# Kernel tuning notes

Hardware: AMD Instinct MI355X
Metric: run time of the kernel (lower is better)

Reference implementation:

```python
import jax, jax.numpy as jnp
import numpy as np

T, B, DIM, N = 2048, 8, 1024, 64

def setup_inputs() -> dict:
    key = jax.random.key(0)
    ks = jax.random.split(key, 6)
    scale = 1.0 / np.sqrt(DIM)  # xavier-ish for Linear(dim, n_state)
    return {
        "x": jax.random.normal(ks[0], (T, B, DIM), dtype=jnp.float32),
        "S0": jnp.zeros((B, N, N), dtype=jnp.float32),
        "W_k": jax.random.normal(ks[1], (N, DIM), dtype=jnp.float32) * scale,
        "W_v": jax.random.normal(ks[2], (N, DIM), dtype=jnp.float32) * scale,
        "W_q": jax.random.normal(ks[3], (N, DIM), dtype=jnp.float32) * scale,
        "W_alpha": jax.random.normal(ks[4], (N, DIM), dtype=jnp.float32) * scale,
        "b_alpha": jnp.full((N,), 2.0, dtype=jnp.float32),
        "d_g": jnp.full((N,), 0.5, dtype=jnp.float32),
        "b_g": jnp.zeros((N,), dtype=jnp.float32),
    }

def reference(x, S0, W_k, W_v, W_q, W_alpha, b_alpha, d_g, b_g):
    # Precompute all projections: [T, B, N]
    k_all = jnp.einsum('tbd,nd->tbn', x, W_k)
    v_all = jnp.einsum('tbd,nd->tbn', x, W_v)
    q_all = jnp.einsum('tbd,nd->tbn', x, W_q)
    alpha_all = jax.nn.sigmoid(jnp.einsum('tbd,nd->tbn', x, W_alpha) + b_alpha)

    def step(S, inp):
        k, v, q, alpha = inp  # each [B, N]
        retrieved = jnp.einsum('bij,bj->bi', S, k)          # S @ k
        g = jax.nn.sigmoid(d_g * retrieved + b_g)
        v_gated = v * g
        outer_vk = jnp.einsum('bi,bj->bij', v_gated, k)
        S = alpha[..., None] * S + (1.0 - alpha[..., None]) * outer_vk
        out = jnp.einsum('bij,bj->bi', S, q)                # S @ q
        out = out * jax.nn.silu(out)                        # self-gate
        return S, out

    S_final, output = jax.lax.scan(step, S0, (k_all, v_all, q_all, alpha_all))
    return output, S_final
```

## Files before the change

kernel.cpp:

```cpp
#include <hip/hip_runtime.h>

#define TT 2048
#define BB 8
#define DD 1024
#define NN 64
#define C64 64
#define NC2 (TT / C64)

typedef __attribute__((ext_vector_type(8))) short bfrag;
typedef __attribute__((ext_vector_type(4))) float f32x4;
typedef __attribute__((ext_vector_type(8))) unsigned short ushort8;

__device__ __forceinline__ float rcp_(float x) { return __builtin_amdgcn_rcpf(x); }
__device__ __forceinline__ float exp2_(float x) {
#if __has_builtin(__builtin_amdgcn_exp2f)
    return __builtin_amdgcn_exp2f(x);
#else
    return exp2f(x);
#endif
}
__device__ __forceinline__ float sigmoidf_(float x) {
    return rcp_(1.0f + __expf(-x));
}
__device__ __forceinline__ float bcastlane(float x, int l) {
    return __int_as_float(__builtin_amdgcn_readlane(__float_as_int(x), l));
}

template <int CTRL, int RM>
__device__ __forceinline__ float dpp_mul1(float x) {
    int v = __builtin_amdgcn_update_dpp(
        0x3f800000, __float_as_int(x), CTRL, RM, 0xF, false);
    return x * __int_as_float(v);
}
__device__ __forceinline__ float prefix_mul64(float x) {
    x = dpp_mul1<0x111, 0xF>(x);
    x = dpp_mul1<0x112, 0xF>(x);
    x = dpp_mul1<0x114, 0xF>(x);
    x = dpp_mul1<0x118, 0xF>(x);
    x = dpp_mul1<0x142, 0xA>(x);
    x = dpp_mul1<0x143, 0xC>(x);
    return x;
}

__device__ __forceinline__ unsigned short cvt_bf16(float f) {
    unsigned int u = __float_as_uint(f);
    return (unsigned short)((u + 0x7FFF + ((u >> 16) & 1)) >> 16);
}

__device__ __forceinline__ void gll16(const float* g, float* l) {
    __builtin_amdgcn_global_load_lds(
        (const __attribute__((address_space(1))) void*)g,
        (__attribute__((address_space(3))) void*)l, 16, 0, 0);
}

__global__ __launch_bounds__(256) void wcvt_kernel(
    const float* __restrict__ W0, const float* __restrict__ W1,
    const float* __restrict__ W2, const float* __restrict__ W3,
    unsigned short* __restrict__ Wb)
{
    const int i = blockIdx.x * 256 + threadIdx.x;
    const int o = i * 8;
    const int col = o & 31;
    const int row = (o >> 5) & 63;
    const int kt  = (o >> 11) & 31;
    const int mat = o >> 16;
    const float* __restrict__ W = (mat == 0) ? W0 : (mat == 1) ? W1
                                 : (mat == 2) ? W2 : W3;
    const float* src = &W[(size_t)row * DD + kt * 32 + col];
    const float4 a = *(const float4*)src;
    const float4 b = *(const float4*)(src + 4);
    ushort8 r;
    r[0] = cvt_bf16(a.x); r[1] = cvt_bf16(a.y);
    r[2] = cvt_bf16(a.z); r[3] = cvt_bf16(a.w);
    r[4] = cvt_bf16(b.x); r[5] = cvt_bf16(b.y);
    r[6] = cvt_bf16(b.z); r[7] = cvt_bf16(b.w);
    *(ushort8*)&Wb[o] = r;
}

__global__ __launch_bounds__(256) void proj_fused_kernel(
    const float* __restrict__ x, const unsigned short* __restrict__ Wb,
    const float* __restrict__ b_alpha,
    float* __restrict__ O0, float* __restrict__ O1,
    float* __restrict__ O2, float* __restrict__ O3)
{
    const int m0   = blockIdx.x * 64;
    const int tid  = threadIdx.x;
    const int lane = tid & 63;
    const int wave = tid >> 6;
    const int ln   = lane & 15;
    const int q8   = (lane >> 4) * 8;

    __shared__ unsigned short As[64][40];
    __shared__ unsigned short Bs[4][64][40];

    f32x4 acc[4][4] = {};

    const int arow = tid >> 2;
    const int aseg = (tid & 3) * 8;

    float4 pa[2];
    ushort8 pw[4];
    {
        const float* ap = &x[(size_t)(m0 + arow) * DD + aseg];
        pa[0] = *(const float4*)ap;
        pa[1] = *(const float4*)(ap + 4);
        const ushort8* wp = (const ushort8*)&Wb[((size_t)(wave * 32 + 0) * 64 + lane) * 32];
        #pragma unroll
        for (int j = 0; j < 4; j++) pw[j] = wp[j];
    }

    for (int k0 = 0; k0 < DD; k0 += 32) {
        __syncthreads();
        {
            unsigned short t8[8];
            const float* pf = (const float*)pa;
            #pragma unroll
            for (int j = 0; j < 8; j++) t8[j] = cvt_bf16(pf[j]);
            *(ushort8*)&As[arow][aseg] = *(ushort8*)&t8[0];
            #pragma unroll
            for (int j = 0; j < 4; j++)
                *(ushort8*)&Bs[wave][lane][8 * j] = pw[j];
        }
        if (k0 + 32 < DD) {
            const int kt = (k0 >> 5) + 1;
            const float* ap = &x[(size_t)(m0 + arow) * DD + k0 + 32 + aseg];
            pa[0] = *(const float4*)ap;
            pa[1] = *(const float4*)(ap + 4);
            const ushort8* wp = (const ushort8*)&Wb[((size_t)(wave * 32 + kt) * 64 + lane) * 32];
            #pragma unroll
            for (int j = 0; j < 4; j++) pw[j] = wp[j];
        }
        __syncthreads();

        const bfrag af = *(const bfrag*)&As[wave * 16 + ln][q8];
        #pragma unroll
        for (int mat = 0; mat < 4; mat++) {
            bfrag bf[4];
            #pragma unroll
            for (int nt = 0; nt < 4; nt++)
                bf[nt] = *(const bfrag*)&Bs[mat][nt * 16 + ln][q8];
            #pragma unroll
            for (int nt = 0; nt < 4; nt++)
                acc[mat][nt] = __builtin_amdgcn_mfma_f32_16x16x32_bf16(
                    af, bf[nt], acc[mat][nt], 0, 0, 0);
        }
    }

    #pragma unroll
    for (int mat = 0; mat < 4; mat++) {
        float* __restrict__ C = (mat == 0) ? O0 : (mat == 1) ? O1
                               : (mat == 2) ? O2 : O3;
        #pragma unroll
        for (int nt = 0; nt < 4; nt++) {
            const int col = nt * 16 + ln;
            const float ba = (mat == 3) ? b_alpha[col] : 0.0f;
            #pragma unroll
            for (int r = 0; r < 4; r++) {
                const int row = m0 + wave * 16 + (lane >> 4) * 4 + r;
                float v = acc[mat][nt][r];
                if (mat == 3) v = sigmoidf_(v + ba);
                C[(size_t)row * NN + col] = v;
            }
        }
    }
}

__global__ __launch_bounds__(256) void gram_kernel(
    const float* __restrict__ k_all, const float* __restrict__ q_all,
    float* __restrict__ gkq)
{
    const int c  = blockIdx.x;
    const int b  = blockIdx.y;
    const int t0 = c * C64;
    const int tid = threadIdx.x;

    __shared__ __align__(16) float Ks[64][68];
    __shared__ __align__(16) float Qs[64][68];

    {
        const int r = tid >> 2, sg = (tid & 3) * 16;
        const float* kp = &k_all[(size_t)(t0 + r) * (BB * NN) + b * NN + sg];
        const float* qp = &q_all[(size_t)(t0 + r) * (BB * NN) + b * NN + sg];
        #pragma unroll
        for (int j = 0; j < 4; ++j) {
            *(float4*)&Ks[r][sg + 4 * j] = *(const float4*)(kp + 4 * j);
            *(float4*)&Qs[r][sg + 4 * j] = *(const float4*)(qp + 4 * j);
        }
    }
    __syncthreads();

    const int ti = tid >> 4, tj = tid & 15;
    float g[4][4] = {}, kq[4][4] = {};
    #pragma unroll
    for (int c4 = 0; c4 < 16; ++c4) {
        float4 ka[4], kb[4], qb[4];
        #pragma unroll
        for (int r = 0; r < 4; ++r) {
            ka[r] = *(const float4*)&Ks[4 * ti + r][c4 * 4];
            kb[r] = *(const float4*)&Ks[4 * tj + r][c4 * 4];
            qb[r] = *(const float4*)&Qs[4 * tj + r][c4 * 4];
        }
        #pragma unroll
        for (int r = 0; r < 4; ++r)
            #pragma unroll
            for (int q = 0; q < 4; ++q) {
                g[r][q]  = fmaf(ka[r].x, kb[q].x, g[r][q]);
                g[r][q]  = fmaf(ka[r].y, kb[q].y, g[r][q]);
                g[r][q]  = fmaf(ka[r].z, kb[q].z, g[r][q]);
                g[r][q]  = fmaf(ka[r].w, kb[q].w, g[r][q]);
                kq[r][q] = fmaf(ka[r].x, qb[q].x, kq[r][q]);
                kq[r][q] = fmaf(ka[r].y, qb[q].y, kq[r][q]);
                kq[r][q] = fmaf(ka[r].z, qb[q].z, kq[r][q]);
                kq[r][q] = fmaf(ka[r].w, qb[q].w, kq[r][q]);
            }
    }

    float* base = gkq + (size_t)(b * NC2 + c) * 64 * 128;
    #pragma unroll
    for (int r = 0; r < 4; ++r) {
        #pragma unroll
        for (int q = 0; q < 4; ++q) {
            const int t   = 4 * tj + q;
            const int pos = ((ti ^ (t & 15)) << 2) + r;
            base[t * 128 + pos]      = g[r][q];
            base[t * 128 + 64 + pos] = kq[r][q];
        }
    }
}

__global__ __launch_bounds__(128, 1) void scan_kernel(
    const float* __restrict__ gkq,
    const float* __restrict__ k_all, const float* __restrict__ q_all,
    const float* __restrict__ a_all, const float* __restrict__ v_all,
    const float* __restrict__ S0,
    const float* __restrict__ d_g, const float* __restrict__ b_g,
    float* __restrict__ out, float* __restrict__ S_final)
{
    const int b    = blockIdx.x;
    const int rg   = blockIdx.y;
    const int tid  = threadIdx.x;
    const int lane = tid & 63;
    const int wave = tid >> 6;
    const int row  = rg * 2 + wave;

    __shared__ __align__(16) float gT[2][64 * 128];
    __shared__ __align__(16) float Kl[2][64 * 64];
    __shared__ __align__(16) float Ql[2][64 * 64];
    __shared__ __align__(16) float sbuf[2][64];

    float S = S0[((size_t)b * NN + row) * NN + lane];
    const float L2E  = 1.4426950408889634f;
    const float ndg2 = -d_g[row] * L2E;
    const float nbg2 = -b_g[row] * L2E;

    const float* gkq_b = gkq + (size_t)b * NC2 * 64 * 128;

    const int s_loc = lane >> 4;
    const int gr    = lane & 15;

    auto stage = [&](int c, int db) {
        const float* src = gkq_b + (size_t)c * 64 * 128;
        #pragma unroll
        for (int j = 0; j < 16; ++j) {
            const int off = (wave * 32 + 2 * j) * 128;
            gll16(src + off + lane * 4, &gT[db][off]);
        }
        #pragma unroll
        for (int j = 0; j < 8; ++j) {
            const int r0 = wave * 32 + 4 * j;
            const int s  = r0 + s_loc;
            const int gg = gr ^ (s & 15);
            const size_t goff = ((size_t)(c * C64 + s) * BB + b) * NN + gg * 4;
            gll16(k_all + goff, &Kl[db][r0 * 64]);
            gll16(q_all + goff, &Ql[db][r0 * 64]);
        }
    };

    float a_nx, v_nx;
    auto aw_load = [&](int c) {
        const size_t goff = ((size_t)(c * C64 + lane) * BB + b) * NN + row;
        a_nx = a_all[goff];
        v_nx = v_all[goff];
    };

    stage(0, 0);
    aw_load(0);

    for (int c = 0; c < NC2; ++c) {
        const int db = c & 1;
        const float ac = a_nx;
        const float wc = (1.0f - a_nx) * v_nx;
        __syncthreads();
        if (c + 1 < NC2) { aw_load(c + 1); stage(c + 1, db ^ 1); }

        const float P  = prefix_mul64(ac);
        const float Pm = P / ac;
        const float u  = wc * rcp_(P);

        sbuf[wave][lane] = S;
        const float* Kb = &Kl[db][0];
        const float* Qb = &Ql[db][0];
        float4 ha = {0.f, 0.f, 0.f, 0.f};
        float4 hb = {0.f, 0.f, 0.f, 0.f};
        #pragma unroll
        for (int g4 = 0; g4 < 16; ++g4) {
            const int idx = lane * 64 + ((g4 ^ gr) << 2);
            float4 kv = *(const float4*)&Kb[idx];
            float4 qv = *(const float4*)&Qb[idx];
            float4 sv = *(const float4*)&sbuf[wave][g4 << 2];
            ha.x = fmaf(kv.x, sv.x, ha.x); ha.y = fmaf(kv.y, sv.y, ha.y);
            ha.z = fmaf(kv.z, sv.z, ha.z); ha.w = fmaf(kv.w, sv.w, ha.w);
            hb.x = fmaf(qv.x, sv.x, hb.x); hb.y = fmaf(qv.y, sv.y, hb.y);
            hb.z = fmaf(qv.z, sv.z, hb.z); hb.w = fmaf(qv.w, sv.w, hb.w);
        }
        const float h  = (ha.x + ha.y) + (ha.z + ha.w);
        const float hq = (hb.x + hb.y) + (hb.z + hb.w);
        const float e1 = ndg2 * Pm;
        const float e0 = fmaf(e1, h, nbg2);

        const float* gt = &gT[db][0];
        const int rowbase = lane * 128;

        float z = e0;
        float Bacc = 0.f, Bl = 0.f, slat = 0.f;

        f32x4 g2a0, g2a1, q2a0, q2a1, g2b0, g2b1, q2b0, q2b1;

#define LOADBLK(G0, G1, Q0, Q1, blk) do {                                   \
        const int j0_ = ((2 * (blk)) ^ gr) << 2;                            \
        const int j1_ = ((2 * (blk) + 1) ^ gr) << 2;                        \
        const f32x4 rg0_ = *(const f32x4*)&gt[rowbase + j0_];               \
        const f32x4 rg1_ = *(const f32x4*)&gt[rowbase + j1_];               \
        const f32x4 rq0_ = *(const f32x4*)&gt[rowbase + 64 + j0_];          \
        const f32x4 rq1_ = *(const f32x4*)&gt[rowbase + 64 + j1_];          \
        const float u0_ = bcastlane(u, 8*(blk)+0);                          \
        const float u1_ = bcastlane(u, 8*(blk)+1);                          \
        const float u2_ = bcastlane(u, 8*(blk)+2);                          \
        const float u3_ = bcastlane(u, 8*(blk)+3);                          \
        const float u4_ = bcastlane(u, 8*(blk)+4);                          \
        const float u5_ = bcastlane(u, 8*(blk)+5);                          \
        const float u6_ = bcastlane(u, 8*(blk)+6);                          \
        const float u7_ = bcastlane(u, 8*(blk)+7);                          \
        Q0[0] = rq0_[0]*u0_; Q0[1] = rq0_[1]*u1_;                           \
        Q0[2] = rq0_[2]*u2_; Q0[3] = rq0_[3]*u3_;                           \
        Q1[0] = rq1_[0]*u4_; Q1[1] = rq1_[1]*u5_;                           \
        Q1[2] = rq1_[2]*u6_; Q1[3] = rq1_[3]*u7_;                           \
        G0[0] = rg0_[0]*u0_*e1; G0[1] = rg0_[1]*u1_*e1;                     \
        G0[2] = rg0_[2]*u2_*e1; G0[3] = rg0_[3]*u3_*e1;                     \
        G1[0] = rg1_[0]*u4_*e1; G1[1] = rg1_[1]*u5_*e1;                     \
        G1[2] = rg1_[2]*u6_*e1; G1[3] = rg1_[3]*u7_*e1;                     \
    } while (0)

#define STEP1(ss, gv, qv) do {                                              \
        const float zs_ = bcastlane(z, (ss));                               \
        const float ex_ = exp2_(zs_);                                       \
        const float sg_ = rcp_(1.0f + ex_);                                 \
        z    = fmaf((gv), sg_, z);                                          \
        Bacc = fmaf((qv), sg_, Bacc);                                       \
        Bl   = (lane == (ss)) ? Bacc : Bl;                                  \
        slat = (lane == (ss)) ? sg_  : slat;                                \
    } while (0)

#define STEP8(blk, G0, G1, Q0, Q1)                                          \
        STEP1(8*(blk)+0, G0[0], Q0[0]); STEP1(8*(blk)+1, G0[1], Q0[1]);     \
        STEP1(8*(blk)+2, G0[2], Q0[2]); STEP1(8*(blk)+3, G0[3], Q0[3]);     \
        STEP1(8*(blk)+4, G1[0], Q1[0]); STEP1(8*(blk)+5, G1[1], Q1[1]);     \
        STEP1(8*(blk)+6, G1[2], Q1[2]); STEP1(8*(blk)+7, G1[3], Q1[3]);

        LOADBLK(g2a0, g2a1, q2a0, q2a1, 0);
        LOADBLK(g2b0, g2b1, q2b0, q2b1, 1);
        STEP8(0, g2a0, g2a1, q2a0, q2a1); LOADBLK(g2a0, g2a1, q2a0, q2a1, 2);
        STEP8(1, g2b0, g2b1, q2b0, q2b1); LOADBLK(g2b0, g2b1, q2b0, q2b1, 3);
        STEP8(2, g2a0, g2a1, q2a0, q2a1); LOADBLK(g2a0, g2a1, q2a0, q2a1, 4);
        STEP8(3, g2b0, g2b1, q2b0, q2b1); LOADBLK(g2b0, g2b1, q2b0, q2b1, 5);
        STEP8(4, g2a0, g2a1, q2a0, q2a1); LOADBLK(g2a0, g2a1, q2a0, q2a1, 6);
        STEP8(5, g2b0, g2b1, q2b0, q2b1); LOADBLK(g2b0, g2b1, q2b0, q2b1, 7);
        STEP8(6, g2a0, g2a1, q2a0, q2a1);
        STEP8(7, g2b0, g2b1, q2b0, q2b1);

#undef LOADBLK
#undef STEP1
#undef STEP8

        const float chl = u * slat;
        float Sa0 = 0.f, Sa1 = 0.f, Sa2 = 0.f, Sa3 = 0.f;
        #pragma unroll
        for (int s = 0; s < 64; s += 4) {
            const float c0 = bcastlane(chl, s);
            const float c1 = bcastlane(chl, s + 1);
            const float c2 = bcastlane(chl, s + 2);
            const float c3 = bcastlane(chl, s + 3);
            const int sw = ((lane >> 2) << 2);
            Sa0 = fmaf(c0, Kb[(s)     * 64 + ((sw ^ (((s)     & 15) << 2))) + (lane & 3)], Sa0);
            Sa1 = fmaf(c1, Kb[(s + 1) * 64 + ((sw ^ (((s + 1) & 15) << 2))) + (lane & 3)], Sa1);
            Sa2 = fmaf(c2, Kb[(s + 2) * 64 + ((sw ^ (((s + 2) & 15) << 2))) + (lane & 3)], Sa2);
            Sa3 = fmaf(c3, Kb[(s + 3) * 64 + ((sw ^ (((s + 3) & 15) << 2))) + (lane & 3)], Sa3);
        }
        const float Sa = (Sa0 + Sa1) + (Sa2 + Sa3);

        const float o = P * (hq + Bl);
        const float y = o * o * rcp_(1.0f + exp2_(-o * L2E));
        out[((size_t)(c * C64 + lane) * BB + b) * NN + row] = y;
        const float Pl = bcastlane(P, 63);
        S = Pl * (S + Sa);
    }

    S_final[((size_t)b * NN + row) * NN + lane] = S;
}

extern "C" void kernel_launch(void* const* d_in, const int* in_sizes, int n_in,
                              void* d_out, int out_size, void* d_ws, size_t ws_size,
                              hipStream_t stream) {
    const float* x       = (const float*)d_in[0];
    const float* S0      = (const float*)d_in[1];
    const float* W_k     = (const float*)d_in[2];
    const float* W_v     = (const float*)d_in[3];
    const float* W_q     = (const float*)d_in[4];
    const float* W_alpha = (const float*)d_in[5];
    const float* b_alpha = (const float*)d_in[6];
    const float* d_g     = (const float*)d_in[7];
    const float* b_g     = (const float*)d_in[8];
    float* out = (float*)d_out;

    const size_t arr = (size_t)TT * BB * NN;
    float* ws    = (float*)d_ws;
    float* k_all = ws;
    float* v_all = ws + arr;
    float* q_all = ws + 2 * arr;
    float* a_all = ws + 3 * arr;
    float* gkq   = ws + 4 * arr;
    unsigned short* Wb = (unsigned short*)(ws + 6 * arr);

    wcvt_kernel<<<dim3(128), 256, 0, stream>>>(W_k, W_v, W_q, W_alpha, Wb);

    proj_fused_kernel<<<dim3(TT * BB / 64), 256, 0, stream>>>(
        x, Wb, b_alpha, k_all, v_all, q_all, a_all);

    gram_kernel<<<dim3(NC2, BB), 256, 0, stream>>>(k_all, q_all, gkq);

    scan_kernel<<<dim3(BB, 32), 128, 0, stream>>>(
        gkq, k_all, q_all, a_all, v_all, S0, d_g, b_g, out, out + arr);
}
```

Measured before the change: 321.4 us.

## Pre-mask causal gram blocks and double-buffer projection LDS tiles

The chunk gram/kq precompute now writes zeros for non-causal entries (s>=t for g, s>t for kq). This lets the scan's serial per-step loop drop the per-lane select tracking of Bacc and the sigmoid value: each lane's final z and Bacc already equal its own causal values, and one extra sigmoid is taken at the end. Separately, the projection GEMM double-buffers its shared-memory A/B tiles so one barrier per k-step replaces two. This costs twice the LDS in the projection kernel and relies on the masking exactly matching the previous lane-select semantics.

```diff
diff --git a/kernel.cpp b/kernel.cpp
--- a/kernel.cpp
+++ b/kernel.cpp
@@ -90,8 +90,8 @@
     const int ln   = lane & 15;
     const int q8   = (lane >> 4) * 8;
 
-    __shared__ unsigned short As[64][40];
-    __shared__ unsigned short Bs[4][64][40];
+    __shared__ unsigned short As[2][64][40];
+    __shared__ unsigned short Bs[2][4][64][40];
 
     f32x4 acc[4][4] = {};
 
@@ -109,36 +109,35 @@
         for (int j = 0; j < 4; j++) pw[j] = wp[j];
     }
 
-    for (int k0 = 0; k0 < DD; k0 += 32) {
-        __syncthreads();
+    for (int kt = 0; kt < 32; ++kt) {
+        const int cur = kt & 1;
         {
             unsigned short t8[8];
             const float* pf = (const float*)pa;
             #pragma unroll
             for (int j = 0; j < 8; j++) t8[j] = cvt_bf16(pf[j]);
-            *(ushort8*)&As[arow][aseg] = *(ushort8*)&t8[0];
+            *(ushort8*)&As[cur][arow][aseg] = *(ushort8*)&t8[0];
             #pragma unroll
             for (int j = 0; j < 4; j++)
-                *(ushort8*)&Bs[wave][lane][8 * j] = pw[j];
-        }
-        if (k0 + 32 < DD) {
-            const int kt = (k0 >> 5) + 1;
-            const float* ap = &x[(size_t)(m0 + arow) * DD + k0 + 32 + aseg];
+                *(ushort8*)&Bs[cur][wave][lane][8 * j] = pw[j];
+        }
+        if (kt + 1 < 32) {
+            const float* ap = &x[(size_t)(m0 + arow) * DD + (kt + 1) * 32 + aseg];
             pa[0] = *(const float4*)ap;
             pa[1] = *(const float4*)(ap + 4);
-            const ushort8* wp = (const ushort8*)&Wb[((size_t)(wave * 32 + kt) * 64 + lane) * 32];
+            const ushort8* wp = (const ushort8*)&Wb[((size_t)(wave * 32 + kt + 1) * 64 + lane) * 32];
             #pragma unroll
             for (int j = 0; j < 4; j++) pw[j] = wp[j];
         }
         __syncthreads();
 
-        const bfrag af = *(const bfrag*)&As[wave * 16 + ln][q8];
+        const bfrag af = *(const bfrag*)&As[cur][wave * 16 + ln][q8];
         #pragma unroll
         for (int mat = 0; mat < 4; mat++) {
             bfrag bf[4];
             #pragma unroll
             for (int nt = 0; nt < 4; nt++)
-                bf[nt] = *(const bfrag*)&Bs[mat][nt * 16 + ln][q8];
+                bf[nt] = *(const bfrag*)&Bs[cur][mat][nt * 16 + ln][q8];
             #pragma unroll
             for (int nt = 0; nt < 4; nt++)
                 acc[mat][nt] = __builtin_amdgcn_mfma_f32_16x16x32_bf16(
@@ -218,12 +217,13 @@
     float* base = gkq + (size_t)(b * NC2 + c) * 64 * 128;
     #pragma unroll
     for (int r = 0; r < 4; ++r) {
+        const int s = 4 * ti + r;
         #pragma unroll
         for (int q = 0; q < 4; ++q) {
             const int t   = 4 * tj + q;
             const int pos = ((ti ^ (t & 15)) << 2) + r;
-            base[t * 128 + pos]      = g[r][q];
-            base[t * 128 + 64 + pos] = kq[r][q];
+            base[t * 128 + pos]      = (s <  t) ? g[r][q]  : 0.0f;
+            base[t * 128 + 64 + pos] = (s <= t) ? kq[r][q] : 0.0f;
         }
     }
 }
@@ -322,7 +322,7 @@
         const int rowbase = lane * 128;
 
         float z = e0;
-        float Bacc = 0.f, Bl = 0.f, slat = 0.f;
+        float Bacc = 0.f;
 
         f32x4 g2a0, g2a1, q2a0, q2a1, g2b0, g2b1, q2b0, q2b1;
 
@@ -353,12 +353,9 @@
 
 #define STEP1(ss, gv, qv) do {                                              \
         const float zs_ = bcastlane(z, (ss));                               \
-        const float ex_ = exp2_(zs_);                                       \
-        const float sg_ = rcp_(1.0f + ex_);                                 \
+        const float sg_ = rcp_(1.0f + exp2_(zs_));                          \
         z    = fmaf((gv), sg_, z);                                          \
         Bacc = fmaf((qv), sg_, Bacc);                                       \
-        Bl   = (lane == (ss)) ? Bacc : Bl;                                  \
-        slat = (lane == (ss)) ? sg_  : slat;                                \
     } while (0)
 
 #define STEP8(blk, G0, G1, Q0, Q1)                                          \
@@ -382,7 +379,9 @@
 #undef STEP1
 #undef STEP8
 
-        const float chl = u * slat;
+        const float sgf = rcp_(1.0f + exp2_(z));
+        const float chl = u * sgf;
+
         float Sa0 = 0.f, Sa1 = 0.f, Sa2 = 0.f, Sa3 = 0.f;
         #pragma unroll
         for (int s = 0; s < 64; s += 4) {
@@ -398,7 +397,7 @@
         }
         const float Sa = (Sa0 + Sa1) + (Sa2 + Sa3);
 
-        const float o = P * (hq + Bl);
+        const float o = P * (hq + Bacc);
         const float y = o * o * rcp_(1.0f + exp2_(-o * L2E));
         out[((size_t)(c * C64 + lane) * BB + b) * NN + row] = y;
         const float Pl = bcastlane(P, 63);
```

Result: faster. 295.1 us (-8.2%).

## Apply causal masking in precomputed Gram tiles and pipeline the sequential sigmoid chain

Applied to the files above, without the earlier changes.

The chunk Gram-matrix kernel now writes zeros for non-causal entries (s>=t for g, s>t for kq). This lets the scan accumulate z and Bacc unconditionally and drop the per-step lane-select bookkeeping for Bl and slat. The sequential intra-chunk recurrence is restructured so the next step's z is computed one step early from broadcast values, taking the sigmoid off the critical dependency chain. The final sigmoid is recomputed from z afterwards. This shortens the serial latency per step but adds extra cross-lane broadcasts and relies on the masked zeros being correct.

```diff
diff --git a/kernel.cpp b/kernel.cpp
--- a/kernel.cpp
+++ b/kernel.cpp
@@ -218,12 +218,13 @@
     float* base = gkq + (size_t)(b * NC2 + c) * 64 * 128;
     #pragma unroll
     for (int r = 0; r < 4; ++r) {
+        const int s = 4 * ti + r;
         #pragma unroll
         for (int q = 0; q < 4; ++q) {
             const int t   = 4 * tj + q;
             const int pos = ((ti ^ (t & 15)) << 2) + r;
-            base[t * 128 + pos]      = g[r][q];
-            base[t * 128 + 64 + pos] = kq[r][q];
+            base[t * 128 + pos]      = (s <  t) ? g[r][q]  : 0.0f;
+            base[t * 128 + 64 + pos] = (s <= t) ? kq[r][q] : 0.0f;
         }
     }
 }
@@ -322,7 +323,7 @@
         const int rowbase = lane * 128;
 
         float z = e0;
-        float Bacc = 0.f, Bl = 0.f, slat = 0.f;
+        float Bacc = 0.f;
 
         f32x4 g2a0, g2a1, q2a0, q2a1, g2b0, g2b1, q2b0, q2b1;
 
@@ -351,38 +352,52 @@
         G1[2] = rg1_[2]*u6_*e1; G1[3] = rg1_[3]*u7_*e1;                     \
     } while (0)
 
-#define STEP1(ss, gv, qv) do {                                              \
-        const float zs_ = bcastlane(z, (ss));                               \
-        const float ex_ = exp2_(zs_);                                       \
-        const float sg_ = rcp_(1.0f + ex_);                                 \
-        z    = fmaf((gv), sg_, z);                                          \
-        Bacc = fmaf((qv), sg_, Bacc);                                       \
-        Bl   = (lane == (ss)) ? Bacc : Bl;                                  \
-        slat = (lane == (ss)) ? sg_  : slat;                                \
-    } while (0)
-
-#define STEP8(blk, G0, G1, Q0, Q1)                                          \
-        STEP1(8*(blk)+0, G0[0], Q0[0]); STEP1(8*(blk)+1, G0[1], Q0[1]);     \
-        STEP1(8*(blk)+2, G0[2], Q0[2]); STEP1(8*(blk)+3, G0[3], Q0[3]);     \
-        STEP1(8*(blk)+4, G1[0], Q1[0]); STEP1(8*(blk)+5, G1[1], Q1[1]);     \
-        STEP1(8*(blk)+6, G1[2], Q1[2]); STEP1(8*(blk)+7, G1[3], Q1[3]);
-
         LOADBLK(g2a0, g2a1, q2a0, q2a1, 0);
         LOADBLK(g2b0, g2b1, q2b0, q2b1, 1);
-        STEP8(0, g2a0, g2a1, q2a0, q2a1); LOADBLK(g2a0, g2a1, q2a0, q2a1, 2);
-        STEP8(1, g2b0, g2b1, q2b0, q2b1); LOADBLK(g2b0, g2b1, q2b0, q2b1, 3);
-        STEP8(2, g2a0, g2a1, q2a0, q2a1); LOADBLK(g2a0, g2a1, q2a0, q2a1, 4);
-        STEP8(3, g2b0, g2b1, q2b0, q2b1); LOADBLK(g2b0, g2b1, q2b0, q2b1, 5);
-        STEP8(4, g2a0, g2a1, q2a0, q2a1); LOADBLK(g2a0, g2a1, q2a0, q2a1, 6);
-        STEP8(5, g2b0, g2b1, q2b0, q2b1); LOADBLK(g2b0, g2b1, q2b0, q2b1, 7);
-        STEP8(6, g2a0, g2a1, q2a0, q2a1);
-        STEP8(7, g2b0, g2b1, q2b0, q2b1);
+
+        float sig = rcp_(1.0f + exp2_(bcastlane(z, 0)));
+        float zn  = fmaf(bcastlane(g2a0[0], 1), sig, bcastlane(z, 1));
+
+#define STEP1(ss, gv, qv, gnv) do {                                         \
+        z    = fmaf((gv), sig, z);                                          \
+        Bacc = fmaf((qv), sig, Bacc);                                       \
+        if ((ss) + 1 < 64) {                                                \
+            const float sn_ = rcp_(1.0f + exp2_(zn));                       \
+            if ((ss) + 2 < 64) {                                            \
+                const float rlz_ = bcastlane(z, (ss) + 2);                  \
+                const float rlg_ = bcastlane((gnv), (ss) + 2);              \
+                zn = fmaf(rlg_, sn_, rlz_);                                 \
+            }                                                               \
+            sig = sn_;                                                      \
+        }                                                                   \
+    } while (0)
+
+#define STEP8(blk, G0, G1, Q0, Q1, NG)                                      \
+        STEP1(8*(blk)+0, G0[0], Q0[0], G0[1]);                              \
+        STEP1(8*(blk)+1, G0[1], Q0[1], G0[2]);                              \
+        STEP1(8*(blk)+2, G0[2], Q0[2], G0[3]);                              \
+        STEP1(8*(blk)+3, G0[3], Q0[3], G1[0]);                              \
+        STEP1(8*(blk)+4, G1[0], Q1[0], G1[1]);                              \
+        STEP1(8*(blk)+5, G1[1], Q1[1], G1[2]);                              \
+        STEP1(8*(blk)+6, G1[2], Q1[2], G1[3]);                              \
+        STEP1(8*(blk)+7, G1[3], Q1[3], NG);
+
+        STEP8(0, g2a0, g2a1, q2a0, q2a1, g2b0[0]); LOADBLK(g2a0, g2a1, q2a0, q2a1, 2);
+        STEP8(1, g2b0, g2b1, q2b0, q2b1, g2a0[0]); LOADBLK(g2b0, g2b1, q2b0, q2b1, 3);
+        STEP8(2, g2a0, g2a1, q2a0, q2a1, g2b0[0]); LOADBLK(g2a0, g2a1, q2a0, q2a1, 4);
+        STEP8(3, g2b0, g2b1, q2b0, q2b1, g2a0[0]); LOADBLK(g2b0, g2b1, q2b0, q2b1, 5);
+        STEP8(4, g2a0, g2a1, q2a0, q2a1, g2b0[0]); LOADBLK(g2a0, g2a1, q2a0, q2a1, 6);
+        STEP8(5, g2b0, g2b1, q2b0, q2b1, g2a0[0]); LOADBLK(g2b0, g2b1, q2b0, q2b1, 7);
+        STEP8(6, g2a0, g2a1, q2a0, q2a1, g2b0[0]);
+        STEP8(7, g2b0, g2b1, q2b0, q2b1, g2b0[0] );
 
 #undef LOADBLK
 #undef STEP1
 #undef STEP8
 
-        const float chl = u * slat;
+        const float sgf = rcp_(1.0f + exp2_(z));
+        const float chl = u * sgf;
+
         float Sa0 = 0.f, Sa1 = 0.f, Sa2 = 0.f, Sa3 = 0.f;
         #pragma unroll
         for (int s = 0; s < 64; s += 4) {
@@ -398,7 +413,7 @@
         }
         const float Sa = (Sa0 + Sa1) + (Sa2 + Sa3);
 
-        const float o = P * (hq + Bl);
+        const float o = P * (hq + Bacc);
         const float y = o * o * rcp_(1.0f + exp2_(-o * L2E));
         out[((size_t)(c * C64 + lane) * BB + b) * NN + row] = y;
         const float Pl = bcastlane(P, 63);
```

After: 304.8 us. 1.05x faster.
